# Optimization experiments

Measured on AMD Instinct MI355X. Metric: run time of the kernel, lower is better.

Reference implementation:

```python
import jax, jax.numpy as jnp
import numpy as np

B, L, D, NH, V, T, CYC = 16, 512, 512, 8, 8000, 17, 2
HD = D // NH


def _attn(q, kv, qw, qb, kw, kb, vw, vb, ow, ob):
    # q: [N, Lq, D], kv: [N, Lk, D]; weights stored [in, out] (= torch W.T)
    N, Lq, _ = q.shape
    Lk = kv.shape[1]
    Q = (q @ qw + qb).reshape(N, Lq, NH, HD)
    K = (kv @ kw + kb).reshape(N, Lk, NH, HD)
    Vv = (kv @ vw + vb).reshape(N, Lk, NH, HD)
    scores = jnp.einsum('nqhd,nkhd->nhqk', Q, K) / np.float32(np.sqrt(HD))
    probs = jax.nn.softmax(scores, axis=-1)
    ctx = jnp.einsum('nhqk,nkhd->nqhd', probs, Vv).reshape(N, Lq, D)
    return ctx @ ow + ob


def _ln(x, w, b, eps=1e-12):
    u = x.mean(-1, keepdims=True)
    s = ((x - u) ** 2).mean(-1, keepdims=True)
    return w * (x - u) / jnp.sqrt(s + eps) + b


def setup_inputs() -> dict:
    key = jax.random.key(0)
    ks = jax.random.split(key, 32)
    p = {}
    p['tokens'] = jax.random.randint(ks[0], (B, L, 1), 0, V)
    p['masks'] = jnp.ones((B, L), dtype=jnp.int64)
    p['heads'] = jax.random.randint(ks[1], (B, L), 0, 2)
    p['tails'] = jax.random.randint(ks[2], (B, L), 0, 2)
    p['char_emb'] = jax.random.normal(ks[3], (V, D), jnp.float32) * 0.02
    i = 4
    for pre in ('sat', 'rel'):
        for nm in ('q', 'k', 'v', 'o'):
            p[f'{pre}_{nm}w'] = jax.random.normal(ks[i], (D, D), jnp.float32) * 0.02
            p[f'{pre}_{nm}b'] = jnp.zeros((D,), jnp.float32)
            i += 1
    p['ln_sat_w'] = jnp.ones((D,), jnp.float32)
    p['ln_sat_b'] = jnp.zeros((D,), jnp.float32)
    p['ln_rel_w'] = jnp.ones((D,), jnp.float32)
    p['ln_rel_b'] = jnp.zeros((D,), jnp.float32)
    p['ofc_w'] = jax.random.normal(ks[i], (D, T), jnp.float32) * 0.02
    p['ofc_b'] = jnp.zeros((T,), jnp.float32)
    return p


def reference(tokens, masks, heads, tails, char_emb,
              sat_qw, sat_qb, sat_kw, sat_kb, sat_vw, sat_vb, sat_ow, sat_ob,
              rel_qw, rel_qb, rel_kw, rel_kb, rel_vw, rel_vb, rel_ow, rel_ob,
              ln_sat_w, ln_sat_b, ln_rel_w, ln_rel_b, ofc_w, ofc_b):
    e = char_emb[tokens[:, :, 0]]  # [B, L, D]
    h = e
    s = e.mean(axis=1)  # relay token [B, D] (avg_pool2d over seq)
    for _ in range(CYC):
        # backward cycle_shift in the source is a correct roll-by-(-1)
        h_last = jnp.roll(h, -1, axis=1)
        # forward cycle_shift in the source is sequential in-place: result[:,0]=h[:,-1],
        # result[:,i>=1]=h[:,0] (the write at i=0 propagates). Reproduced faithfully.
        h_next = jnp.concatenate(
            [h[:, -1:, :], jnp.broadcast_to(h[:, :1, :], (B, L - 1, D))], axis=1)
        sm = jnp.broadcast_to(s[:, None, :], (B, L, D))
        c = jnp.stack([h_last, h, h_next, e, sm], axis=2).reshape(B * L, 5, D)
        hq = h.reshape(B * L, 1, D)
        a = _attn(hq, c, sat_qw, sat_qb, sat_kw, sat_kb, sat_vw, sat_vb, sat_ow, sat_ob)
        h = _ln(jax.nn.relu(a), ln_sat_w, ln_sat_b).reshape(B, L, D)
        mc = jnp.concatenate([s[:, None, :], h], axis=1)  # [B, L+1, D]
        r = _attn(s[:, None, :], mc, rel_qw, rel_qb, rel_kw, rel_kb, rel_vw, rel_vb, rel_ow, rel_ob)
        s = _ln(jax.nn.relu(r), ln_rel_w, ln_rel_b)[:, 0, :]
    logits = h @ ofc_w + ofc_b  # [B, L, T]
    return logits
```

## Files before the change

### kernel.cpp

```cpp
#include <hip/hip_runtime.h>
#include <hip/hip_bf16.h>

typedef __hip_bfloat16 bf16;

#define BB 16
#define LL 512
#define DD 512
#define NHH 8
#define HDD 64
#define TT 17
#define MM (BB*LL)
#define RCH 8
#define RCK 65

typedef __attribute__((ext_vector_type(8))) short bfrag;
typedef __attribute__((ext_vector_type(4))) float ffrag;
typedef __attribute__((ext_vector_type(8))) unsigned short us8;

struct Params {
  const int* tokens;
  const float* emb;
  const float *sat_qw, *sat_qb, *sat_kw, *sat_kb, *sat_vw, *sat_vb, *sat_ow, *sat_ob;
  const float *rel_qw, *rel_qb, *rel_kw, *rel_kb, *rel_vw, *rel_vb, *rel_ow, *rel_ob;
  const float *ln_sat_w, *ln_sat_b, *ln_rel_w, *ln_rel_b, *ofc_w, *ofc_b;
  bf16 *ebf, *qkv, *kvbuf, *KeVe, *qbuf, *ctxbf, *WtAll, *WtO, *WtLog;
  float *s, *KsVs, *qr, *Ksr, *Vsr, *mpart, *pws, *out;
};

static __device__ __forceinline__ void gld16(const void* g, void* l){
  __builtin_amdgcn_global_load_lds((const __attribute__((address_space(1))) void*)g,
                                   (__attribute__((address_space(3))) void*)l, 16, 0, 0);
}
static __device__ __forceinline__ float us2f(unsigned short u){
  unsigned int v = ((unsigned int)u) << 16;
  float f; __builtin_memcpy(&f, &v, 4); return f;
}
static __device__ __forceinline__ float hsum8(float v){
  v += __shfl_xor(v, 1); v += __shfl_xor(v, 2); v += __shfl_xor(v, 4);
  return v;
}

__global__ __launch_bounds__(256) void k_init(Params P){
  __shared__ __align__(16) char sm[8192];
  int u = blockIdx.x, t = threadIdx.x;
  if (u < 256){
    int* toks = (int*)sm;
    int b = u >> 4, lc = u & 15;
    if (t < 32) toks[t] = P.tokens[b*LL + lc*32 + t];
    __syncthreads();
    bf16* eb = P.ebf + ((size_t)b*LL + lc*32)*DD;
    for (int d = t; d < DD; d += 256){
      float acc = 0.f;
      #pragma unroll 4
      for (int l = 0; l < 32; l++){
        float v = P.emb[(size_t)toks[l]*DD + d];
        eb[(size_t)l*DD + d] = __float2bfloat16(v);
        acc += v;
      }
      P.mpart[(size_t)u*DD + d] = acc;
    }
    return;
  }
  int w = u - 256;
  int z = w >> 8, xy = w & 255;
  int tx = t & 31, ty = t >> 5;
  if (z == 6){
    int i = (xy << 8) + t;
    int row = i >> 9, k = i & 511;
    P.WtLog[i] = __float2bfloat16(row < TT ? P.ofc_w[(size_t)k*TT + row] : 0.f);
    return;
  }
  float (*tile)[33] = (float(*)[33])sm;
  const float* in = (z==0)?P.sat_qw:(z==1)?P.sat_kw:(z==2)?P.sat_vw:
                    (z==3)?P.rel_kw:(z==4)?P.rel_vw:P.sat_ow;
  bf16* out = (z<5) ? (P.WtAll + (size_t)z*512*512) : P.WtO;
  int bx = (xy & 15)*32, by = (xy >> 4)*32;
  #pragma unroll
  for (int j = 0; j < 32; j += 8)
    tile[ty + j][tx] = in[(size_t)(by + ty + j)*DD + bx + tx];
  __syncthreads();
  #pragma unroll
  for (int j = 0; j < 32; j += 8)
    out[(size_t)(bx + ty + j)*DD + by + tx] = __float2bfloat16(tile[tx][ty + j]);
}

__global__ __launch_bounds__(256)
void k_sproj0(Params P){
  __shared__ float sL[16][512];
  __shared__ float part[8][32][17];
  int t = threadIdx.x;
  for (int o = t; o < 8192; o += 256){
    int m = o >> 9, d = o & 511;
    float a = 0.f;
    #pragma unroll
    for (int c = 0; c < 16; c++) a += P.mpart[(size_t)(m*16 + c)*DD + d];
    sL[m][d] = a * (1.0f/LL);
  }
  __syncthreads();
  int n = t & 31, kg = t >> 5;
  int wi = blockIdx.x >> 4, ch = blockIdx.x & 15;
  const float* W  = (wi==0)?P.sat_kw:(wi==1)?P.sat_vw:(wi==2)?P.rel_qw:
                    (wi==3)?P.rel_kw:P.rel_vw;
  const float* bs = (wi==0)?P.sat_kb:(wi==1)?P.sat_vb:(wi==2)?P.rel_qb:
                    (wi==3)?P.rel_kb:P.rel_vb;
  float* O  = (wi==0)?P.KsVs:(wi==1)?(P.KsVs+512):(wi==2)?P.qr:(wi==3)?P.Ksr:P.Vsr;
  int ldc   = (wi<2) ? 1024 : 512;
  int col = ch*32 + n;
  float acc[16];
  #pragma unroll
  for (int m = 0; m < 16; m++) acc[m] = 0.f;
  const float* Wp = W + (size_t)(kg*64)*512 + col;
  for (int k = 0; k < 64; k++){
    float w = Wp[(size_t)k*512];
    int kk = kg*64 + k;
    #pragma unroll
    for (int m = 0; m < 16; m++) acc[m] = fmaf(sL[m][kk], w, acc[m]);
  }
  #pragma unroll
  for (int m = 0; m < 16; m++) part[kg][n][m] = acc[m];
  __syncthreads();
  for (int o = t; o < 512; o += 256){
    int m = o >> 5, nn = o & 31;
    float v = 0.f;
    #pragma unroll
    for (int g = 0; g < 8; g++) v += part[g][nn][m];
    O[(size_t)m*ldc + ch*32 + nn] = v + bs[ch*32 + nn];
  }
}

__global__ __launch_bounds__(256)
void k_sproj1(Params P){
  __shared__ float part[8][32][17];
  int t = threadIdx.x;
  int n = t & 31, kg = t >> 5;
  int wi = blockIdx.x >> 4, ch = blockIdx.x & 15;
  const float* W  = (wi==0)?P.sat_kw:P.sat_vw;
  const float* bs = (wi==0)?P.sat_kb:P.sat_vb;
  float* O  = (wi==0)?P.KsVs:(P.KsVs+512);
  int col = ch*32 + n;
  float acc[16];
  #pragma unroll
  for (int m = 0; m < 16; m++) acc[m] = 0.f;
  const float* Wp = W + (size_t)(kg*64)*512 + col;
  const float* Ap = P.s + kg*64;
  for (int k = 0; k < 64; k++){
    float w = Wp[(size_t)k*512];
    #pragma unroll
    for (int m = 0; m < 16; m++) acc[m] = fmaf(Ap[m*512 + k], w, acc[m]);
  }
  #pragma unroll
  for (int m = 0; m < 16; m++) part[kg][n][m] = acc[m];
  __syncthreads();
  for (int o = t; o < 512; o += 256){
    int m = o >> 5, nn = o & 31;
    float v = 0.f;
    #pragma unroll
    for (int g = 0; g < 8; g++) v += part[g][nn][m];
    O[(size_t)m*1024 + ch*32 + nn] = v + bs[ch*32 + nn];
  }
}

__global__ __launch_bounds__(256)
void k_gemm(Params P, const bf16* __restrict__ A, const bf16* __restrict__ Wt,
            const float* b0, const float* b1, const float* b2, const float* b3,
            const float* b4,
            bf16* D0, int ld0, bf16* D1, int ld1, int split){
  const int K = 512;
  __shared__ bf16 As[128*32];
  __shared__ bf16 Bs[128*32];
  int t = threadIdx.x;
  int wave = t >> 6, lane = t & 63;
  int id = blockIdx.x;
  int bm = (((id & 7) << 3) | ((id >> 3) & 7)) * 128;
  int bn = (id >> 6) * 128;
  int wm = (wave & 1) * 64, wn = (wave >> 1) * 64;
  ffrag acc[4][4];
  #pragma unroll
  for (int i = 0; i < 4; i++)
    #pragma unroll
    for (int j = 0; j < 4; j++) acc[i][j] = (ffrag){0.f,0.f,0.f,0.f};

  int srow = t >> 2;
  int scol = ((((t & 3) - ((t >> 3) & 3)) & 3)) * 8;
  const bf16* gA = A  + (size_t)(bm + srow)*K + scol;
  const bf16* gB = Wt + (size_t)(bn + srow)*K + scol;
  char* lA = (char*)As + 16*t;
  char* lB = (char*)Bs + 16*t;
  int q = lane >> 4, r = lane & 15;
  int cs = (((q + (r >> 1)) & 3)) * 8;

  for (int k0 = 0; k0 < K; k0 += 32){
    gld16(gA + k0,          lA);
    gld16(gA + 64*K + k0,   lA + 4096);
    gld16(gB + k0,          lB);
    gld16(gB + 64*K + k0,   lB + 4096);
    __syncthreads();
    bfrag af[4], bfv[4];
    #pragma unroll
    for (int i = 0; i < 4; i++){
      af[i]  = *(const bfrag*)(As + (wm + i*16 + r)*32 + cs);
      bfv[i] = *(const bfrag*)(Bs + (wn + i*16 + r)*32 + cs);
    }
    #pragma unroll
    for (int i = 0; i < 4; i++)
      #pragma unroll
      for (int j = 0; j < 4; j++)
        acc[i][j] = __builtin_amdgcn_mfma_f32_16x16x32_bf16(af[i], bfv[j], acc[i][j], 0, 0, 0);
    __syncthreads();
  }
  #pragma unroll
  for (int i = 0; i < 4; i++){
    #pragma unroll
    for (int j = 0; j < 4; j++){
      int row = bm + wm + i*16 + q*4;
      int col = bn + wn + j*16 + r;
      const float* bp = (col < 512) ? b0 : (col < 1024) ? b1 :
                        (col < 1536) ? b2 : (col < 2048) ? b3 : b4;
      float bias = bp[col & 511];
      bf16* D; int ld;
      if (col < split){ D = D0 + (size_t)row*ld0 + col;         ld = ld0; }
      else            { D = D1 + (size_t)row*ld1 + (col-split); ld = ld1; }
      #pragma unroll
      for (int g = 0; g < 4; g++)
        D[(size_t)g*ld] = __float2bfloat16(acc[i][j][g] + bias);
    }
  }
}

__global__ __launch_bounds__(256) void k_logits(Params P){
  const int K = 512;
  __shared__ bf16 As[128*32];
  __shared__ bf16 Bs[128*32];
  int t = threadIdx.x;
  int wave = t >> 6, lane = t & 63;
  int bm = blockIdx.x * 128;
  int wm = wave * 32;
  ffrag acc[2][2];
  #pragma unroll
  for (int i = 0; i < 2; i++){ acc[i][0] = (ffrag){0,0,0,0}; acc[i][1] = (ffrag){0,0,0,0}; }
  int srow = t >> 2;
  int scol = ((((t & 3) - ((t >> 3) & 3)) & 3)) * 8;
  const bf16* gA = P.ebf + (size_t)(bm + srow)*K + scol;
  const bf16* gB = P.WtLog + (size_t)srow*K + scol;
  char* lA = (char*)As + 16*t;
  char* lB = (char*)Bs + 16*t;
  int q = lane >> 4, r = lane & 15;
  int cs = (((q + (r >> 1)) & 3)) * 8;

  for (int k0 = 0; k0 < K; k0 += 32){
    gld16(gA + k0,          lA);
    gld16(gA + 64*K + k0,   lA + 4096);
    gld16(gB + k0,          lB);
    gld16(gB + 64*K + k0,   lB + 4096);
    __syncthreads();
    bfrag bf0 = *(const bfrag*)(Bs + (r)*32 + cs);
    bfrag bf1 = *(const bfrag*)(Bs + (16 + r)*32 + cs);
    #pragma unroll
    for (int i = 0; i < 2; i++){
      bfrag af = *(const bfrag*)(As + (wm + i*16 + r)*32 + cs);
      acc[i][0] = __builtin_amdgcn_mfma_f32_16x16x32_bf16(af, bf0, acc[i][0], 0, 0, 0);
      acc[i][1] = __builtin_amdgcn_mfma_f32_16x16x32_bf16(af, bf1, acc[i][1], 0, 0, 0);
    }
    __syncthreads();
  }
  #pragma unroll
  for (int i = 0; i < 2; i++)
    #pragma unroll
    for (int j = 0; j < 2; j++){
      int row = bm + wm + i*16 + q*4;
      int col = j*16 + r;
      if (col < TT){
        float bv = P.ofc_b[col];
        #pragma unroll
        for (int g = 0; g < 4; g++)
          P.out[(size_t)(row + g)*TT + col] = acc[i][j][g] + bv;
      }
    }
}

__global__ __launch_bounds__(256)
void k_sat(Params P, const bf16* qp, int sq, const bf16* kp, const bf16* vp, int skv){
  int tok = blockIdx.x*4 + (threadIdx.x >> 6);
  int l = threadIdx.x & 63;
  int b = tok >> 9, li = tok & 511;
  int off = l*8;
  int t0 = (b << 9) | ((li + 1) & 511);
  int t2 = (b << 9) | (li == 0 ? 511 : 0);
  float qf[8];
  { us8 q8 = *(const us8*)(qp + (size_t)tok*sq + off);
    #pragma unroll
    for (int g = 0; g < 8; g++) qf[g] = us2f(q8[g]); }
  float sc[5];
  int rows[3] = {t0, tok, t2};
  #pragma unroll
  for (int j = 0; j < 3; j++){
    us8 k8 = *(const us8*)(kp + (size_t)rows[j]*skv + off);
    float a = 0.f;
    #pragma unroll
    for (int g = 0; g < 8; g++) a += qf[g]*us2f(k8[g]);
    sc[j] = hsum8(a) * 0.125f;
  }
  { us8 k8 = *(const us8*)(P.KeVe + (size_t)tok*1024 + off);
    float a = 0.f;
    #pragma unroll
    for (int g = 0; g < 8; g++) a += qf[g]*us2f(k8[g]);
    sc[3] = hsum8(a) * 0.125f; }
  { const float* ks = P.KsVs + (size_t)b*1024 + off;
    float4 f0 = *(const float4*)ks, f1 = *(const float4*)(ks + 4);
    float a = qf[0]*f0.x + qf[1]*f0.y + qf[2]*f0.z + qf[3]*f0.w
            + qf[4]*f1.x + qf[5]*f1.y + qf[6]*f1.z + qf[7]*f1.w;
    sc[4] = hsum8(a) * 0.125f; }
  float m = fmaxf(fmaxf(fmaxf(sc[0],sc[1]), fmaxf(sc[2],sc[3])), sc[4]);
  float pr[5], den = 0.f;
  #pragma unroll
  for (int j = 0; j < 5; j++){ pr[j] = __expf(sc[j]-m); den += pr[j]; }
  float inv = 1.0f/den;
  float o[8];
  #pragma unroll
  for (int g = 0; g < 8; g++) o[g] = 0.f;
  #pragma unroll
  for (int j = 0; j < 3; j++){
    us8 v8 = *(const us8*)(vp + (size_t)rows[j]*skv + off);
    #pragma unroll
    for (int g = 0; g < 8; g++) o[g] += pr[j]*us2f(v8[g]);
  }
  { us8 v8 = *(const us8*)(P.KeVe + (size_t)tok*1024 + 512 + off);
    #pragma unroll
    for (int g = 0; g < 8; g++) o[g] += pr[3]*us2f(v8[g]); }
  { const float* vs = P.KsVs + (size_t)b*1024 + 512 + off;
    float4 f0 = *(const float4*)vs, f1 = *(const float4*)(vs + 4);
    o[0] += pr[4]*f0.x; o[1] += pr[4]*f0.y; o[2] += pr[4]*f0.z; o[3] += pr[4]*f0.w;
    o[4] += pr[4]*f1.x; o[5] += pr[4]*f1.y; o[6] += pr[4]*f1.z; o[7] += pr[4]*f1.w; }
  bf16 ob[8];
  #pragma unroll
  for (int g = 0; g < 8; g++) ob[g] = __float2bfloat16(o[g]*inv);
  *(us8*)(P.ctxbf + (size_t)tok*DD + off) = *(const us8*)ob;
}

__global__ __launch_bounds__(256) void k_ln(Params P, const bf16* X, bf16* Y){
  int row = blockIdx.x*4 + (threadIdx.x >> 6);
  int lane = threadIdx.x & 63;
  int off = lane*8;
  us8 x8 = *(const us8*)(X + (size_t)row*DD + off);
  float v[8], sum = 0.f;
  #pragma unroll
  for (int g = 0; g < 8; g++){ v[g] = fmaxf(us2f(x8[g]), 0.f); sum += v[g]; }
  #pragma unroll
  for (int o = 32; o; o >>= 1) sum += __shfl_xor(sum, o);
  float u = sum * (1.0f/DD);
  float d[8], var = 0.f;
  #pragma unroll
  for (int g = 0; g < 8; g++){ d[g] = v[g] - u; var += d[g]*d[g]; }
  #pragma unroll
  for (int o = 32; o; o >>= 1) var += __shfl_xor(var, o);
  float inv = rsqrtf(var * (1.0f/DD) + 1e-12f);
  bf16 ob[8];
  #pragma unroll
  for (int g = 0; g < 8; g++)
    ob[g] = __float2bfloat16(P.ln_sat_w[off+g]*d[g]*inv + P.ln_sat_b[off+g]);
  *(us8*)(Y + (size_t)row*DD + off) = *(const us8*)ob;
}

__global__ __launch_bounds__(256) void k_relp(Params P){
  __shared__ __align__(16) char sm[4096];
  int u = blockIdx.x, t = threadIdx.x;
  int ch = u & 7, hh = (u >> 3) & 7, b = u >> 6;
  float* qs   = (float*)sm;
  float* sc   = (float*)(sm + 256);
  float* red  = (float*)(sm + 1024);
  float (*part)[64] = (float(*)[64])(sm + 2048);
  int base = hh * HDD;
  int j0 = ch * RCK;
  int nk = min(513 - j0, RCK);
  if (t < 64) qs[t] = P.qr[(size_t)b*DD + base + t];
  __syncthreads();
  if (t < nk){
    int j = j0 + t;
    float a = 0.f;
    if (j == 0){
      const float* kr = P.Ksr + (size_t)b*DD + base;
      #pragma unroll
      for (int d = 0; d < 64; d += 4){
        float4 k4 = *(const float4*)(kr + d);
        float4 q4 = *(const float4*)(qs + d);
        a += q4.x*k4.x + q4.y*k4.y + q4.z*k4.z + q4.w*k4.w;
      }
    } else {
      const bf16* kr = P.kvbuf + ((size_t)b*LL + j - 1)*1024 + base;
      #pragma unroll
      for (int d = 0; d < 64; d += 8){
        us8 k8 = *(const us8*)(kr + d);
        #pragma unroll
        for (int g = 0; g < 8; g++) a += qs[d+g] * us2f(k8[g]);
      }
    }
    sc[t] = a * 0.125f;
  }
  __syncthreads();
  red[t] = (t < nk) ? sc[t] : -1e30f; __syncthreads();
  for (int st = 128; st; st >>= 1){ if (t < st) red[t] = fmaxf(red[t], red[t+st]); __syncthreads(); }
  float m = red[0]; __syncthreads();
  if (t < nk) sc[t] = __expf(sc[t] - m);
  __syncthreads();
  red[t] = (t < nk) ? sc[t] : 0.f; __syncthreads();
  for (int st = 128; st; st >>= 1){ if (t < st) red[t] += red[t+st]; __syncthreads(); }
  float l = red[0];
  int d = t & 63, c2 = t >> 6;
  float a = 0.f;
  for (int j = c2; j < nk; j += 4){
    int gj = j0 + j;
    float vv = (gj == 0) ? P.Vsr[(size_t)b*DD + base + d]
                         : __bfloat162float(P.kvbuf[((size_t)b*LL + gj - 1)*1024 + 512 + base + d]);
    a += sc[j] * vv;
  }
  part[c2][d] = a; __syncthreads();
  float* o = P.pws + (((size_t)(b*NHH + hh))*RCH + ch) * 66;
  if (t < 64) o[t] = part[0][t] + part[1][t] + part[2][t] + part[3][t];
  else if (t == 64) o[64] = m;
  else if (t == 65) o[65] = l;
}

__global__ __launch_bounds__(256) void k_reltail2(Params P){
  __shared__ float crs[512];
  __shared__ float part[8][33];
  int b = blockIdx.x >> 4, ch = blockIdx.x & 15;
  int t = threadIdx.x;
  for (int o = t; o < 512; o += 256){
    int hh = o >> 6, d = o & 63;
    const float* p = P.pws + ((size_t)(b*NHH + hh))*RCH*66;
    float M = -1e30f;
    #pragma unroll
    for (int c = 0; c < RCH; c++) M = fmaxf(M, p[c*66 + 64]);
    float den = 0.f, acc = 0.f;
    #pragma unroll
    for (int c = 0; c < RCH; c++){
      float w = __expf(p[c*66 + 64] - M);
      den += w * p[c*66 + 65];
      acc += w * p[c*66 + d];
    }
    crs[o] = acc / den;
  }
  __syncthreads();
  int n = t & 31, kg = t >> 5;
  int col = ch*32 + n;
  const float* Wp = P.rel_ow + (size_t)(kg*64)*512 + col;
  const float* cp = crs + kg*64;
  float a = 0.f;
  for (int k = 0; k < 64; k++) a = fmaf(cp[k], Wp[(size_t)k*512], a);
  part[kg][n] = a;
  __syncthreads();
  if (t < 32){
    float v = P.rel_ob[ch*32 + t];
    #pragma unroll
    for (int g = 0; g < 8; g++) v += part[g][t];
    P.qr[(size_t)b*DD + ch*32 + t] = v;
  }
}

__global__ __launch_bounds__(256) void k_lnrel(Params P){
  int row = blockIdx.x*4 + (threadIdx.x >> 6);
  int lane = threadIdx.x & 63;
  int off = lane*8;
  const float* x = P.qr + (size_t)row*DD + off;
  float4 f0 = *(const float4*)x, f1 = *(const float4*)(x + 4);
  float v[8] = {f0.x, f0.y, f0.z, f0.w, f1.x, f1.y, f1.z, f1.w};
  float sum = 0.f;
  #pragma unroll
  for (int g = 0; g < 8; g++){ v[g] = fmaxf(v[g], 0.f); sum += v[g]; }
  #pragma unroll
  for (int o = 32; o; o >>= 1) sum += __shfl_xor(sum, o);
  float u = sum * (1.0f/DD);
  float d[8], var = 0.f;
  #pragma unroll
  for (int g = 0; g < 8; g++){ d[g] = v[g] - u; var += d[g]*d[g]; }
  #pragma unroll
  for (int o = 32; o; o >>= 1) var += __shfl_xor(var, o);
  float inv = rsqrtf(var * (1.0f/DD) + 1e-12f);
  #pragma unroll
  for (int g = 0; g < 8; g++)
    P.s[(size_t)row*DD + off + g] = P.ln_rel_w[off+g]*d[g]*inv + P.ln_rel_b[off+g];
}

extern "C" void kernel_launch(void* const* d_in, const int* in_sizes, int n_in,
                              void* d_out, int out_size, void* d_ws, size_t ws_size,
                              hipStream_t stream) {
  Params P;
  P.tokens  = (const int*)  d_in[0];
  P.emb     = (const float*)d_in[4];
  P.sat_qw  = (const float*)d_in[5];  P.sat_qb = (const float*)d_in[6];
  P.sat_kw  = (const float*)d_in[7];  P.sat_kb = (const float*)d_in[8];
  P.sat_vw  = (const float*)d_in[9];  P.sat_vb = (const float*)d_in[10];
  P.sat_ow  = (const float*)d_in[11]; P.sat_ob = (const float*)d_in[12];
  P.rel_qw  = (const float*)d_in[13]; P.rel_qb = (const float*)d_in[14];
  P.rel_kw  = (const float*)d_in[15]; P.rel_kb = (const float*)d_in[16];
  P.rel_vw  = (const float*)d_in[17]; P.rel_vb = (const float*)d_in[18];
  P.rel_ow  = (const float*)d_in[19]; P.rel_ob = (const float*)d_in[20];
  P.ln_sat_w= (const float*)d_in[21]; P.ln_sat_b= (const float*)d_in[22];
  P.ln_rel_w= (const float*)d_in[23]; P.ln_rel_b= (const float*)d_in[24];
  P.ofc_w   = (const float*)d_in[25]; P.ofc_b  = (const float*)d_in[26];

  char* p = (char*)d_ws;
  auto alloc = [&](size_t bytes) -> char* {
    char* r = p; p += (bytes + 255) & ~(size_t)255; return r;
  };
  const size_t BIGH = (size_t)MM*DD*2;
  P.ebf   = (bf16*) alloc(BIGH);
  P.qkv   = (bf16*) alloc(3*BIGH);
  P.kvbuf = (bf16*) alloc(2*BIGH);
  P.KeVe  = (bf16*) alloc(2*BIGH);
  P.qbuf  = (bf16*) alloc(BIGH);
  P.ctxbf = (bf16*) alloc(BIGH);
  P.WtAll = (bf16*) alloc((size_t)2560*512*2);
  P.WtO   = (bf16*) alloc((size_t)512*512*2);
  P.WtLog = (bf16*) alloc((size_t)128*512*2);
  P.s     = (float*)alloc(BB*DD*4);
  P.KsVs  = (float*)alloc(BB*1024*4);
  P.qr    = (float*)alloc(BB*DD*4);
  P.Ksr   = (float*)alloc(BB*DD*4);
  P.Vsr   = (float*)alloc(BB*DD*4);
  P.mpart = (float*)alloc((size_t)256*DD*4);
  P.pws   = (float*)alloc((size_t)BB*NHH*RCH*66*4);
  P.out   = (float*)d_out;

  bf16* hbf  = P.ebf;
  bf16* aout = P.qkv;

  k_init<<<2048, 256, 0, stream>>>(P);
  k_sproj0<<<80, 256, 0, stream>>>(P);
  k_gemm<<<768, 256, 0, stream>>>(P, P.ebf, P.WtAll,
      P.sat_qb, P.sat_kb, P.sat_vb, P.sat_vb, P.sat_vb, P.qbuf, 512, P.KeVe, 1024, 512);
  k_sat<<<MM/4, 256, 0, stream>>>(P, P.qbuf, 512, P.KeVe, P.KeVe + 512, 1024);
  k_gemm<<<256, 256, 0, stream>>>(P, P.ctxbf, P.WtO,
      P.sat_ob, P.sat_ob, P.sat_ob, P.sat_ob, P.sat_ob, aout, 512, aout, 512, 512);
  k_ln<<<MM/4, 256, 0, stream>>>(P, aout, hbf);
  k_gemm<<<1280, 256, 0, stream>>>(P, hbf, P.WtAll,
      P.sat_qb, P.sat_kb, P.sat_vb, P.rel_kb, P.rel_vb, P.qkv, 1536, P.kvbuf, 1024, 1536);
  k_relp<<<BB*NHH*RCH, 256, 0, stream>>>(P);
  k_reltail2<<<256, 256, 0, stream>>>(P);
  k_lnrel<<<4, 256, 0, stream>>>(P);
  k_sproj1<<<32, 256, 0, stream>>>(P);
  k_sat<<<MM/4, 256, 0, stream>>>(P, P.qkv, 1536, P.qkv + 512, P.qkv + 1024, 1536);
  k_gemm<<<256, 256, 0, stream>>>(P, P.ctxbf, P.WtO,
      P.sat_ob, P.sat_ob, P.sat_ob, P.sat_ob, P.sat_ob, aout, 512, aout, 512, 512);
  k_ln<<<MM/4, 256, 0, stream>>>(P, aout, hbf);
  k_logits<<<64, 256, 0, stream>>>(P);
}
```

Before: 305.2 us.

## Fuse small kernels to cut launches: mean via atomics, merged GEMM, last-block LN

Computes the relay mean by atomically adding per-chunk sums into s, which removes the mpart buffer and its reduction pass. The initial QKV GEMM and the small s-projections now share one launch. The relay LayerNorm moves into the last finishing block of k_reltail2, found with a per-batch atomic counter, and the final LayerNorm is fused into the start of k_logits. The aim is fewer kernel launches and less time on serial tails. The cost is atomic float ordering nondeterminism, a memset, and redundant LN loads in the logits kernel.

```diff
diff --git a/kernel.cpp b/kernel.cpp
--- a/kernel.cpp
+++ b/kernel.cpp
@@ -24,7 +24,8 @@
   const float *rel_qw, *rel_qb, *rel_kw, *rel_kb, *rel_vw, *rel_vb, *rel_ow, *rel_ob;
   const float *ln_sat_w, *ln_sat_b, *ln_rel_w, *ln_rel_b, *ofc_w, *ofc_b;
   bf16 *ebf, *qkv, *kvbuf, *KeVe, *qbuf, *ctxbf, *WtAll, *WtO, *WtLog;
-  float *s, *KsVs, *qr, *Ksr, *Vsr, *mpart, *pws, *out;
+  float *s, *KsVs, *qr, *Ksr, *Vsr, *pws, *out;
+  int* cnt;
 };
 
 static __device__ __forceinline__ void gld16(const void* g, void* l){
@@ -57,7 +58,7 @@
         eb[(size_t)l*DD + d] = __float2bfloat16(v);
         acc += v;
       }
-      P.mpart[(size_t)u*DD + d] = acc;
+      atomicAdd(&P.s[(size_t)b*DD + d], acc * (1.0f/LL));
     }
     return;
   }
@@ -85,20 +86,74 @@
 }
 
 __global__ __launch_bounds__(256)
-void k_sproj0(Params P){
-  __shared__ float sL[16][512];
-  __shared__ float part[8][32][17];
+void k_qkvsp(Params P){
+  __shared__ __align__(16) char smu[17408];
   int t = threadIdx.x;
-  for (int o = t; o < 8192; o += 256){
-    int m = o >> 9, d = o & 511;
-    float a = 0.f;
-    #pragma unroll
-    for (int c = 0; c < 16; c++) a += P.mpart[(size_t)(m*16 + c)*DD + d];
-    sL[m][d] = a * (1.0f/LL);
-  }
-  __syncthreads();
+  if (blockIdx.x < 768){
+    const int K = 512;
+    bf16* As = (bf16*)smu;
+    bf16* Bs = (bf16*)(smu + 8192);
+    const bf16* __restrict__ A  = P.ebf;
+    const bf16* __restrict__ Wt = P.WtAll;
+    int wave = t >> 6, lane = t & 63;
+    int id = blockIdx.x;
+    int bm = (((id & 7) << 3) | ((id >> 3) & 7)) * 128;
+    int bn = (id >> 6) * 128;
+    int wm = (wave & 1) * 64, wn = (wave >> 1) * 64;
+    ffrag acc[4][4];
+    #pragma unroll
+    for (int i = 0; i < 4; i++)
+      #pragma unroll
+      for (int j = 0; j < 4; j++) acc[i][j] = (ffrag){0.f,0.f,0.f,0.f};
+    int srow = t >> 2;
+    int scol = ((((t & 3) - ((t >> 3) & 3)) & 3)) * 8;
+    const bf16* gA = A  + (size_t)(bm + srow)*K + scol;
+    const bf16* gB = Wt + (size_t)(bn + srow)*K + scol;
+    char* lA = (char*)As + 16*t;
+    char* lB = (char*)Bs + 16*t;
+    int q = lane >> 4, r = lane & 15;
+    int cs = (((q + (r >> 1)) & 3)) * 8;
+    for (int k0 = 0; k0 < K; k0 += 32){
+      gld16(gA + k0,          lA);
+      gld16(gA + 64*K + k0,   lA + 4096);
+      gld16(gB + k0,          lB);
+      gld16(gB + 64*K + k0,   lB + 4096);
+      __syncthreads();
+      bfrag af[4], bfv[4];
+      #pragma unroll
+      for (int i = 0; i < 4; i++){
+        af[i]  = *(const bfrag*)(As + (wm + i*16 + r)*32 + cs);
+        bfv[i] = *(const bfrag*)(Bs + (wn + i*16 + r)*32 + cs);
+      }
+      #pragma unroll
+      for (int i = 0; i < 4; i++)
+        #pragma unroll
+        for (int j = 0; j < 4; j++)
+          acc[i][j] = __builtin_amdgcn_mfma_f32_16x16x32_bf16(af[i], bfv[j], acc[i][j], 0, 0, 0);
+      __syncthreads();
+    }
+    #pragma unroll
+    for (int i = 0; i < 4; i++){
+      #pragma unroll
+      for (int j = 0; j < 4; j++){
+        int row = bm + wm + i*16 + q*4;
+        int col = bn + wn + j*16 + r;
+        const float* bp = (col < 512) ? P.sat_qb : (col < 1024) ? P.sat_kb : P.sat_vb;
+        float bias = bp[col & 511];
+        bf16* D; int ld;
+        if (col < 512){ D = P.qbuf + (size_t)row*512 + col;        ld = 512; }
+        else          { D = P.KeVe + (size_t)row*1024 + (col-512); ld = 1024; }
+        #pragma unroll
+        for (int g = 0; g < 4; g++)
+          D[(size_t)g*ld] = __float2bfloat16(acc[i][j][g] + bias);
+      }
+    }
+    return;
+  }
+  float (*part)[32][17] = (float(*)[32][17])smu;
+  int u = blockIdx.x - 768;
   int n = t & 31, kg = t >> 5;
-  int wi = blockIdx.x >> 4, ch = blockIdx.x & 15;
+  int wi = u >> 4, ch = u & 15;
   const float* W  = (wi==0)?P.sat_kw:(wi==1)?P.sat_vw:(wi==2)?P.rel_qw:
                     (wi==3)?P.rel_kw:P.rel_vw;
   const float* bs = (wi==0)?P.sat_kb:(wi==1)?P.sat_vb:(wi==2)?P.rel_qb:
@@ -106,18 +161,18 @@
   float* O  = (wi==0)?P.KsVs:(wi==1)?(P.KsVs+512):(wi==2)?P.qr:(wi==3)?P.Ksr:P.Vsr;
   int ldc   = (wi<2) ? 1024 : 512;
   int col = ch*32 + n;
-  float acc[16];
-  #pragma unroll
-  for (int m = 0; m < 16; m++) acc[m] = 0.f;
+  float acc2[16];
+  #pragma unroll
+  for (int m = 0; m < 16; m++) acc2[m] = 0.f;
   const float* Wp = W + (size_t)(kg*64)*512 + col;
+  const float* Ap = P.s + kg*64;
   for (int k = 0; k < 64; k++){
     float w = Wp[(size_t)k*512];
-    int kk = kg*64 + k;
-    #pragma unroll
-    for (int m = 0; m < 16; m++) acc[m] = fmaf(sL[m][kk], w, acc[m]);
-  }
-  #pragma unroll
-  for (int m = 0; m < 16; m++) part[kg][n][m] = acc[m];
+    #pragma unroll
+    for (int m = 0; m < 16; m++) acc2[m] = fmaf(Ap[m*512 + k], w, acc2[m]);
+  }
+  #pragma unroll
+  for (int m = 0; m < 16; m++) part[kg][n][m] = acc2[m];
   __syncthreads();
   for (int o = t; o < 512; o += 256){
     int m = o >> 5, nn = o & 31;
@@ -234,6 +289,33 @@
   int t = threadIdx.x;
   int wave = t >> 6, lane = t & 63;
   int bm = blockIdx.x * 128;
+  {
+    const bf16* aout = P.qkv;
+    bf16* hbf = P.ebf;
+    int off = lane*8;
+    for (int rr = 0; rr < 32; rr++){
+      int row = bm + wave*32 + rr;
+      us8 x8 = *(const us8*)(aout + (size_t)row*DD + off);
+      float v[8], sum = 0.f;
+      #pragma unroll
+      for (int g = 0; g < 8; g++){ v[g] = fmaxf(us2f(x8[g]), 0.f); sum += v[g]; }
+      #pragma unroll
+      for (int o = 32; o; o >>= 1) sum += __shfl_xor(sum, o);
+      float u = sum * (1.0f/DD);
+      float d[8], var = 0.f;
+      #pragma unroll
+      for (int g = 0; g < 8; g++){ d[g] = v[g] - u; var += d[g]*d[g]; }
+      #pragma unroll
+      for (int o = 32; o; o >>= 1) var += __shfl_xor(var, o);
+      float inv = rsqrtf(var * (1.0f/DD) + 1e-12f);
+      bf16 ob[8];
+      #pragma unroll
+      for (int g = 0; g < 8; g++)
+        ob[g] = __float2bfloat16(P.ln_sat_w[off+g]*d[g]*inv + P.ln_sat_b[off+g]);
+      *(us8*)(hbf + (size_t)row*DD + off) = *(const us8*)ob;
+    }
+  }
+  __syncthreads();
   int wm = wave * 32;
   ffrag acc[2][2];
   #pragma unroll
@@ -423,6 +505,7 @@
 __global__ __launch_bounds__(256) void k_reltail2(Params P){
   __shared__ float crs[512];
   __shared__ float part[8][33];
+  __shared__ int lastFlag;
   int b = blockIdx.x >> 4, ch = blockIdx.x & 15;
   int t = threadIdx.x;
   for (int o = t; o < 512; o += 256){
@@ -453,32 +536,24 @@
     float v = P.rel_ob[ch*32 + t];
     #pragma unroll
     for (int g = 0; g < 8; g++) v += part[g][t];
-    P.qr[(size_t)b*DD + ch*32 + t] = v;
-  }
-}
-
-__global__ __launch_bounds__(256) void k_lnrel(Params P){
-  int row = blockIdx.x*4 + (threadIdx.x >> 6);
-  int lane = threadIdx.x & 63;
-  int off = lane*8;
-  const float* x = P.qr + (size_t)row*DD + off;
-  float4 f0 = *(const float4*)x, f1 = *(const float4*)(x + 4);
-  float v[8] = {f0.x, f0.y, f0.z, f0.w, f1.x, f1.y, f1.z, f1.w};
-  float sum = 0.f;
-  #pragma unroll
-  for (int g = 0; g < 8; g++){ v[g] = fmaxf(v[g], 0.f); sum += v[g]; }
-  #pragma unroll
-  for (int o = 32; o; o >>= 1) sum += __shfl_xor(sum, o);
-  float u = sum * (1.0f/DD);
-  float d[8], var = 0.f;
-  #pragma unroll
-  for (int g = 0; g < 8; g++){ d[g] = v[g] - u; var += d[g]*d[g]; }
-  #pragma unroll
-  for (int o = 32; o; o >>= 1) var += __shfl_xor(var, o);
-  float inv = rsqrtf(var * (1.0f/DD) + 1e-12f);
-  #pragma unroll
-  for (int g = 0; g < 8; g++)
-    P.s[(size_t)row*DD + off + g] = P.ln_rel_w[off+g]*d[g]*inv + P.ln_rel_b[off+g];
+    atomicExch(&P.qr[(size_t)b*DD + ch*32 + t], v);
+  }
+  __syncthreads();
+  if (t == 0) lastFlag = (atomicAdd(&P.cnt[b], 1) == 15);
+  __syncthreads();
+  if (!lastFlag) return;
+  float v0 = atomicAdd(&P.qr[(size_t)b*DD + t],       0.0f);
+  float v1 = atomicAdd(&P.qr[(size_t)b*DD + t + 256], 0.0f);
+  float w0 = fmaxf(v0, 0.f), w1 = fmaxf(v1, 0.f);
+  crs[t] = w0 + w1; __syncthreads();
+  for (int st = 128; st; st >>= 1){ if (t < st) crs[t] += crs[t+st]; __syncthreads(); }
+  float u = crs[0] * (1.0f/DD); __syncthreads();
+  float d0 = w0 - u, d1 = w1 - u;
+  crs[t] = d0*d0 + d1*d1; __syncthreads();
+  for (int st = 128; st; st >>= 1){ if (t < st) crs[t] += crs[t+st]; __syncthreads(); }
+  float inv = rsqrtf(crs[0] * (1.0f/DD) + 1e-12f);
+  P.s[(size_t)b*DD + t]       = P.ln_rel_w[t]    *d0*inv + P.ln_rel_b[t];
+  P.s[(size_t)b*DD + t + 256] = P.ln_rel_w[t+256]*d1*inv + P.ln_rel_b[t+256];
 }
 
 extern "C" void kernel_launch(void* const* d_in, const int* in_sizes, int n_in,
@@ -514,21 +589,21 @@
   P.WtO   = (bf16*) alloc((size_t)512*512*2);
   P.WtLog = (bf16*) alloc((size_t)128*512*2);
   P.s     = (float*)alloc(BB*DD*4);
+  P.cnt   = (int*)  alloc(64);
   P.KsVs  = (float*)alloc(BB*1024*4);
   P.qr    = (float*)alloc(BB*DD*4);
   P.Ksr   = (float*)alloc(BB*DD*4);
   P.Vsr   = (float*)alloc(BB*DD*4);
-  P.mpart = (float*)alloc((size_t)256*DD*4);
   P.pws   = (float*)alloc((size_t)BB*NHH*RCH*66*4);
   P.out   = (float*)d_out;
 
   bf16* hbf  = P.ebf;
   bf16* aout = P.qkv;
 
+  hipMemsetAsync(P.s, 0, BB*DD*4 + 64, stream);
+
   k_init<<<2048, 256, 0, stream>>>(P);
-  k_sproj0<<<80, 256, 0, stream>>>(P);
-  k_gemm<<<768, 256, 0, stream>>>(P, P.ebf, P.WtAll,
-      P.sat_qb, P.sat_kb, P.sat_vb, P.sat_vb, P.sat_vb, P.qbuf, 512, P.KeVe, 1024, 512);
+  k_qkvsp<<<848, 256, 0, stream>>>(P);
   k_sat<<<MM/4, 256, 0, stream>>>(P, P.qbuf, 512, P.KeVe, P.KeVe + 512, 1024);
   k_gemm<<<256, 256, 0, stream>>>(P, P.ctxbf, P.WtO,
       P.sat_ob, P.sat_ob, P.sat_ob, P.sat_ob, P.sat_ob, aout, 512, aout, 512, 512);
@@ -537,11 +612,9 @@
       P.sat_qb, P.sat_kb, P.sat_vb, P.rel_kb, P.rel_vb, P.qkv, 1536, P.kvbuf, 1024, 1536);
   k_relp<<<BB*NHH*RCH, 256, 0, stream>>>(P);
   k_reltail2<<<256, 256, 0, stream>>>(P);
-  k_lnrel<<<4, 256, 0, stream>>>(P);
   k_sproj1<<<32, 256, 0, stream>>>(P);
   k_sat<<<MM/4, 256, 0, stream>>>(P, P.qkv, 1536, P.qkv + 512, P.qkv + 1024, 1536);
   k_gemm<<<256, 256, 0, stream>>>(P, P.ctxbf, P.WtO,
       P.sat_ob, P.sat_ob, P.sat_ob, P.sat_ob, P.sat_ob, aout, 512, aout, 512, 512);
-  k_ln<<<MM/4, 256, 0, stream>>>(P, aout, hbf);
   k_logits<<<64, 256, 0, stream>>>(P);
 }
```

New measurement: 326.7 us. 1.07x slower.
